# Kernel optimization log

Hardware: AMD Instinct MI355X
Metric: run time of the kernel (lower is better)

## Reference

```python
import jax, jax.numpy as jnp
import numpy as np

B, C, N, F_IN = 8, 5, 512, 768
H, D_HID, D_OUT = 4, 128, 64
NEG_SLOPE = 0.2


def _gat_layer(h, mask, W, a_l, a_r, b, apply_relu):
    # h: [B,N,Fin], mask: [B,N,N] bool (mask[b,i,j]=True means edge i->j)
    Bn, Nn, _ = h.shape
    Hh, Dd = a_l.shape
    feat = (h @ W).reshape(Bn, Nn, Hh, Dd)              # [B,N,H,D]
    el = jnp.einsum('bnhd,hd->bnh', feat, a_l)          # src scores
    er = jnp.einsum('bnhd,hd->bnh', feat, a_r)          # dst scores
    e = jax.nn.leaky_relu(el[:, :, None, :] + er[:, None, :, :], NEG_SLOPE)  # [B,src,dst,H]
    m = mask[..., None]
    e = jnp.where(m, e, jnp.finfo(e.dtype).min)
    emax = jnp.max(e, axis=1, keepdims=True)
    p = jnp.where(m, jnp.exp(e - emax), 0.0)
    s = jnp.sum(p, axis=1, keepdims=True)
    alpha = p / jnp.maximum(s, 1e-9)                    # edge softmax over incoming edges per dst
    out = jnp.einsum('bijh,bihd->bjhd', alpha, feat)    # aggregate src features to dst
    out = out + b.reshape(1, 1, Hh, Dd)
    if apply_relu:
        out = jax.nn.relu(out)
    return out                                           # [B,N,H,D]


def setup_inputs() -> dict:
    key = jax.random.key(0)
    ks = jax.random.split(key, 16)
    x = jax.random.normal(ks[0], (B, C, N, F_IN), dtype=jnp.float32)
    adj = (jax.random.uniform(ks[1], (B, C, N, N)) < 0.1).astype(jnp.float32)
    node_nums = jnp.full((B,), N, dtype=jnp.int32)
    s = 0.02
    W0 = jax.random.normal(ks[2], (C, F_IN, H * D_HID)) * s
    al0 = jax.random.normal(ks[3], (C, H, D_HID)) * s
    ar0 = jax.random.normal(ks[4], (C, H, D_HID)) * s
    b0 = jnp.zeros((C, H * D_HID), jnp.float32)
    W1 = jax.random.normal(ks[5], (C, H * D_HID, H * D_HID)) * s
    al1 = jax.random.normal(ks[6], (C, H, D_HID)) * s
    ar1 = jax.random.normal(ks[7], (C, H, D_HID)) * s
    b1 = jnp.zeros((C, H * D_HID), jnp.float32)
    W2 = jax.random.normal(ks[8], (C, H * D_HID, H * D_OUT)) * s
    al2 = jax.random.normal(ks[9], (C, H, D_OUT)) * s
    ar2 = jax.random.normal(ks[10], (C, H, D_OUT)) * s
    b2 = jnp.zeros((C, H * D_OUT), jnp.float32)
    return dict(x=x, adj=adj, W0=W0, al0=al0, ar0=ar0, b0=b0,
                W1=W1, al1=al1, ar1=ar1, b1=b1,
                W2=W2, al2=al2, ar2=ar2, b2=b2, node_nums=node_nums)


def reference(x, adj, W0, al0, ar0, b0, W1, al1, ar1, b1, W2, al2, ar2, b2, node_nums):
    # Original concatenates per-batch node slices and takes channel 0 features only.
    h0 = x[:, 0]                       # [B,N,F_IN]
    logits_all = []
    for c in range(C):
        mask = adj[:, c] > 0           # [B,N,N]
        h = _gat_layer(h0, mask, W0[c], al0[c], ar0[c], b0[c].reshape(H, D_HID), True).reshape(B, N, H * D_HID)
        h = _gat_layer(h, mask, W1[c], al1[c], ar1[c], b1[c].reshape(H, D_HID), True).reshape(B, N, H * D_HID)
        out = _gat_layer(h, mask, W2[c], al2[c], ar2[c], b2[c].reshape(H, D_OUT), False).mean(axis=2)  # [B,N,D_OUT]
        logits_all.append(out)
    return jnp.concatenate(logits_all, axis=-1)  # [B,N,C*D_OUT]
```

## Files before the change

kernel.cpp:

```cpp
#include <hip/hip_runtime.h>

typedef unsigned int uint;
typedef unsigned short ushort_t;
typedef __attribute__((ext_vector_type(8))) short short8;
typedef __attribute__((ext_vector_type(4))) float f32x4;

#define NB 8
#define NC 5
#define NN 512
#define FIN 768
#define NH 4
#define MT 4096

__device__ __forceinline__ float b2f(ushort_t u){ uint x = ((uint)u)<<16; return __builtin_bit_cast(float, x); }
__device__ __forceinline__ ushort_t f2b(float f){
  uint u = __builtin_bit_cast(uint, f);
  u += 0x7FFFu + ((u>>16)&1u);
  return (ushort_t)(u>>16);
}
__device__ __forceinline__ ushort_t f2b_fast(float f){
  uint u = __builtin_bit_cast(uint, f);
  return (ushort_t)((u + 0x8000u)>>16);
}

#define GLL16(gp, lp) __builtin_amdgcn_global_load_lds( \
    (const __attribute__((address_space(1))) void*)(gp), \
    (__attribute__((address_space(3))) void*)(lp), 16, 0, 0)

__global__ __launch_bounds__(256) void prep(const float* __restrict__ x, ushort_t* __restrict__ h0b,
                                            const float* __restrict__ W0, ushort_t* __restrict__ Wt0,
                                            const float* __restrict__ W1, ushort_t* __restrict__ Wt1,
                                            const float* __restrict__ W2, ushort_t* __restrict__ Wt2,
                                            const float* __restrict__ adj, uint* __restrict__ adjB){
  __shared__ float tile[32][33];
  int bid = blockIdx.x, t = threadIdx.x;
  if (bid < 3072){
    int tid = bid*256 + t;
    int row = tid/192, q = tid%192;
    int b = row >> 9, n = row & 511;
    float4 v = *(const float4*)(x + ((size_t)(b*NC)*NN + n)*FIN + q*4);
    ushort4 o; o.x = f2b(v.x); o.y = f2b(v.y); o.z = f2b(v.z); o.w = f2b(v.w);
    *(ushort4*)(h0b + (size_t)row*FIN + q*4) = o;
  } else if (bid < 6912){
    const float* W; ushort_t* Wt; int K, N, c, x0, y0;
    if (bid < 4992){ int l = bid-3072; K=768; N=512; W=W0; Wt=Wt0; c=l/384; int r=l%384; x0=r%16; y0=r/16; }
    else if (bid < 6272){ int l = bid-4992; K=512; N=512; W=W1; Wt=Wt1; c=l/256; int r=l%256; x0=r%16; y0=r/16; }
    else { int l = bid-6272; K=512; N=256; W=W2; Wt=Wt2; c=l/128; int r=l%128; x0=r%8; y0=r/8; }
    int n0 = x0*32, k0 = y0*32;
    int tx = t & 31, ty = t >> 5;
    const float* Wp = W + (size_t)c*K*N;
    ushort_t* Wtp = Wt + (size_t)c*K*N;
    #pragma unroll
    for (int r=0;r<4;r++) tile[ty+r*8][tx] = Wp[(size_t)(k0+ty+r*8)*N + n0+tx];
    __syncthreads();
    #pragma unroll
    for (int r=0;r<4;r++) Wtp[(size_t)(n0+ty+r*8)*K + k0+tx] = f2b(tile[tx][ty+r*8]);
  } else {
    int l = bid - 6912;
    int iw = l & 15, zz = l >> 4;
    const float* ap = adj + (size_t)zz*NN*NN + (size_t)iw*32*NN;
    uint w0 = 0, w1 = 0;
    #pragma unroll 8
    for (int q=0;q<32;q++){
      if (ap[(size_t)q*NN + t]       > 0.f) w0 |= (1u<<q);
      if (ap[(size_t)q*NN + t + 256] > 0.f) w1 |= (1u<<q);
    }
    adjB[((size_t)zz*16 + iw)*512 + t]       = w0;
    adjB[((size_t)zz*16 + iw)*512 + t + 256] = w1;
  }
}

template<int DH>
__global__ __launch_bounds__(256) void gemm_tn(const ushort_t* __restrict__ A,
                                               const ushort_t* __restrict__ Bt,
                                               ushort_t* __restrict__ Ob,
                                               const float* __restrict__ al, const float* __restrict__ ar,
                                               float* __restrict__ el, float* __restrict__ E1, float* __restrict__ E2,
                                               float* __restrict__ er, float* __restrict__ R1, float* __restrict__ R2,
                                               int K, long a_cs, long b_cs){
  constexpr int DT = NH*DH;
  __shared__ __align__(16) char smem[128*136*2];
  __shared__ float als_s[128], ars_s[128];
  ushort_t* As = (ushort_t*)smem;
  ushort_t* Bs = As + 128*32;
  ushort_t* St = (ushort_t*)smem;
  int c = blockIdx.z;
  const ushort_t* Ap = A + (size_t)c*a_cs;
  const ushort_t* Bp = Bt + (size_t)c*b_cs;
  int m0 = blockIdx.y*128, n0 = blockIdx.x*128;
  int t = threadIdx.x, lane = t & 63, w = t >> 6;
  int l15 = lane & 15, quad = lane >> 4;
  int wm = (w & 1)*64, wn = (w >> 1)*64;
  if (t < 128){
    als_s[t] = al[(size_t)c*NH*DH + n0 + t];
    ars_s[t] = ar[(size_t)c*NH*DH + n0 + t];
  }
  f32x4 acc[4][4] = {};
  for (int k0 = 0; k0 < K; k0 += 32){
    __syncthreads();
    {
      int i = t;
      GLL16(Ap + (size_t)(m0 + (i>>2))*K + k0 + (i&3)*8, As + (size_t)(w*64)*8);
      GLL16(Bp + (size_t)(n0 + (i>>2))*K + k0 + (i&3)*8, Bs + (size_t)(w*64)*8);
      i = t + 256;
      GLL16(Ap + (size_t)(m0 + (i>>2))*K + k0 + (i&3)*8, As + (size_t)(w*64 + 256)*8);
      GLL16(Bp + (size_t)(n0 + (i>>2))*K + k0 + (i&3)*8, Bs + (size_t)(w*64 + 256)*8);
    }
    __syncthreads();
    short8 af[4], bfr[4];
    #pragma unroll
    for (int im=0; im<4; im++) af[im] = *(const short8*)(As + (size_t)(wm + im*16 + l15)*32 + quad*8);
    #pragma unroll
    for (int in=0; in<4; in++) bfr[in] = *(const short8*)(Bs + (size_t)(wn + in*16 + l15)*32 + quad*8);
    #pragma unroll
    for (int im=0; im<4; im++)
      #pragma unroll
      for (int in=0; in<4; in++)
        acc[im][in] = __builtin_amdgcn_mfma_f32_16x16x32_bf16(af[im], bfr[in], acc[im][in], 0, 0, 0);
  }
  __syncthreads();
  #pragma unroll
  for (int im=0; im<4; im++)
    #pragma unroll
    for (int in=0; in<4; in++){
      int n = wn + in*16 + l15;
      #pragma unroll
      for (int r=0; r<4; r++){
        int m = wm + im*16 + quad*4 + r;
        St[(size_t)n*136 + m] = f2b(acc[im][in][r]);
      }
    }
  __syncthreads();
  {
    int n_loc = t >> 1, half = t & 1;
    const ushort_t* srcp = St + (size_t)n_loc*136 + half*64;
    ushort_t* dstc = Ob + (size_t)c*MT*DT;
    #pragma unroll
    for (int q=0;q<8;q++){
      size_t g = (size_t)(m0>>3) + half*8 + q;
      *(short8*)(dstc + (g*DT + n0 + n_loc)*8) = *(const short8*)(srcp + q*8);
    }
  }
  {
    int m = t >> 1, half = t & 1;
    float sl = 0.f, sr = 0.f;
    const ushort_t* stp = St + (size_t)(half*64)*136 + m;
    #pragma unroll 8
    for (int nn=0; nn<64; nn++){
      float f = b2f(stp[(size_t)nn*136]);
      int n = half*64 + nn;
      sl += f*als_s[n]; sr += f*ars_s[n];
    }
    size_t base = (size_t)c*NH*MT;
    if (DH == 128){
      sl += __shfl_xor(sl, 1); sr += __shfl_xor(sr, 1);
      size_t idx = base + (size_t)(n0>>7)*MT + m0 + m;
      if (half == 0){ el[idx]=sl; E1[idx]=__expf(sl); E2[idx]=__expf(0.2f*sl); }
      else          { er[idx]=sr; R1[idx]=__expf(sr); R2[idx]=__expf(0.2f*sr); }
    } else {
      size_t idx = base + (size_t)((n0>>6)+half)*MT + m0 + m;
      el[idx]=sl; E1[idx]=__expf(sl); E2[idx]=__expf(0.2f*sl);
      er[idx]=sr; R1[idx]=__expf(sr); R2[idx]=__expf(0.2f*sr);
    }
  }
}

template<int DH, int RELU>
__global__ __launch_bounds__(256,4) void agg(const ushort_t* __restrict__ featB,
                                             const uint* __restrict__ adjB,
                                             const float* __restrict__ el, const float* __restrict__ E1,
                                             const float* __restrict__ E2,
                                             const float* __restrict__ er, const float* __restrict__ R1,
                                             const float* __restrict__ R2,
                                             const float* __restrict__ bias,
                                             ushort_t* __restrict__ outp){
  constexpr int DT = NH*DH;
  constexpr int BN = DH/16;
  __shared__ __align__(16) ushort_t Fs[2][8*DH*8];
  __shared__ float el_s[512], E1_s[512], E2_s[512];
  int bid = blockIdx.x;
  int g = bid % 160, jt = bid / 160;
  int c = g>>5, b = (g>>2)&7, h = g&3;
  int zz = b*NC + c;
  int j0 = jt*64;
  int t = threadIdx.x, lane = t&63, w = t>>6, l15 = lane&15, quad = lane>>4;
  size_t eb = (size_t)(c*NH + h)*MT + b*NN;
  const ushort_t* fBc = featB + ((size_t)(c*512 + b*64)*DT + h*DH)*8;
  el_s[t] = el[eb + t]; el_s[t+256] = el[eb + t+256];
  E1_s[t] = E1[eb + t]; E1_s[t+256] = E1[eb + t+256];
  E2_s[t] = E2[eb + t]; E2_s[t+256] = E2[eb + t+256];
  int jme = j0 + w*16 + l15;
  float erv = er[eb + jme];
  float R1v = R1[eb + jme];
  float R2v = R2[eb + jme];
  uint mw[16];
  #pragma unroll
  for (int iw=0; iw<16; iw++) mw[iw] = adjB[((size_t)zz*16 + iw)*512 + jme];
  short8 onesv;
  #pragma unroll
  for (int q=0;q<8;q++) onesv[q] = (short)0x3F80;
  f32x4 acc[BN] = {};
  f32x4 accs = {0.f,0.f,0.f,0.f};
  #pragma unroll
  for (int u=0; u<DH/32; u++){
    int gi = w*(DH/32)+u, isub = gi/(DH/64), part = gi%(DH/64);
    GLL16(fBc + (size_t)isub*DT*8 + part*512 + lane*8, &Fs[0][isub*(DH*8) + part*512]);
  }
  __syncthreads();
  for (int ic = 0; ic < 8; ic++){
    int buf = ic & 1;
    if (ic < 7){
      #pragma unroll
      for (int u=0; u<DH/32; u++){
        int gi = w*(DH/32)+u, isub = gi/(DH/64), part = gi%(DH/64);
        GLL16(fBc + (size_t)((ic+1)*8+isub)*DT*8 + part*512 + lane*8, &Fs[buf^1][isub*(DH*8) + part*512]);
      }
    }
    #pragma unroll
    for (int st=0; st<2; st++){
      int i0c = ic*64 + st*32;
      uint mby = (mw[i0c>>5] >> (quad*8)) & 0xFFu;
      float4 ea  = *(const float4*)&el_s[i0c + quad*8];
      float4 eb4 = *(const float4*)&el_s[i0c + quad*8 + 4];
      float4 x1a = *(const float4*)&E1_s[i0c + quad*8];
      float4 x1b = *(const float4*)&E1_s[i0c + quad*8 + 4];
      float4 x2a = *(const float4*)&E2_s[i0c + quad*8];
      float4 x2b = *(const float4*)&E2_s[i0c + quad*8 + 4];
      float ev[8]  = {ea.x,ea.y,ea.z,ea.w,eb4.x,eb4.y,eb4.z,eb4.w};
      float e1v[8] = {x1a.x,x1a.y,x1a.z,x1a.w,x1b.x,x1b.y,x1b.z,x1b.w};
      float e2v[8] = {x2a.x,x2a.y,x2a.z,x2a.w,x2b.x,x2b.y,x2b.z,x2b.w};
      short8 af;
      #pragma unroll
      for (int q=0;q<8;q++){
        float s = ev[q] + erv;
        float p = (s > 0.f) ? (e1v[q]*R1v) : (e2v[q]*R2v);
        p = ((mby>>q)&1u) ? p : 0.f;
        af[q] = (short)f2b_fast(p);
      }
      accs = __builtin_amdgcn_mfma_f32_16x16x32_bf16(af, onesv, accs, 0, 0, 0);
      #pragma unroll
      for (int in=0; in<BN; in++){
        short8 bfr = *(const short8*)&Fs[buf][(st*4+quad)*(DH*8) + (in*16+l15)*8];
        acc[in] = __builtin_amdgcn_mfma_f32_16x16x32_bf16(af, bfr, acc[in], 0, 0, 0);
      }
    }
    __syncthreads();
  }
  ushort_t* op = outp + ((size_t)c*MT + b*NN + j0 + w*16)*DT + h*DH;
  float bv[BN];
  #pragma unroll
  for (int in=0; in<BN; in++) bv[in] = bias[(size_t)c*DT + h*DH + in*16 + l15];
  #pragma unroll
  for (int r=0; r<4; r++){
    int jr = quad*4 + r;
    float sinv = 1.f / fmaxf(accs[r], 1e-9f);
    #pragma unroll
    for (int in=0; in<BN; in++){
      float o = acc[in][r]*sinv + bv[in];
      if (RELU) o = fmaxf(o, 0.f);
      op[(size_t)jr*DT + in*16 + l15] = f2b_fast(o);
    }
  }
}

__global__ __launch_bounds__(256) void meank(const ushort_t* __restrict__ h2, float* __restrict__ outp){
  int tid = blockIdx.x*256 + threadIdx.x;
  if (tid >= MT*NC*64) return;
  int d = tid & 63; int r = tid >> 6; int c = r % NC; int m = r / NC;
  const ushort_t* p = h2 + ((size_t)c*MT + m)*256 + d;
  float s = 0.25f*(b2f(p[0]) + b2f(p[64]) + b2f(p[128]) + b2f(p[192]));
  outp[(size_t)m*(NC*64) + c*64 + d] = s;
}

extern "C" void kernel_launch(void* const* d_in, const int* in_sizes, int n_in,
                              void* d_out, int out_size, void* d_ws, size_t ws_size,
                              hipStream_t stream){
  const float* x   = (const float*)d_in[0];
  const float* adj = (const float*)d_in[1];
  const float* W0  = (const float*)d_in[2];
  const float* al0 = (const float*)d_in[3];
  const float* ar0 = (const float*)d_in[4];
  const float* b0  = (const float*)d_in[5];
  const float* W1  = (const float*)d_in[6];
  const float* al1 = (const float*)d_in[7];
  const float* ar1 = (const float*)d_in[8];
  const float* b1  = (const float*)d_in[9];
  const float* W2  = (const float*)d_in[10];
  const float* al2 = (const float*)d_in[11];
  const float* ar2 = (const float*)d_in[12];
  const float* b2  = (const float*)d_in[13];

  ushort_t* h0b  = (ushort_t*)d_ws;
  ushort_t* Wt0  = h0b  + (size_t)MT*FIN;
  ushort_t* Wt1  = Wt0  + (size_t)5*512*768;
  ushort_t* Wt2  = Wt1  + (size_t)5*512*512;
  ushort_t* featB= Wt2  + (size_t)5*256*512;
  ushort_t* hnat = featB+ (size_t)5*(size_t)MT*512;
  uint*     adjB = (uint*)(hnat + (size_t)5*(size_t)MT*512);
  float*    elp  = (float*)(adjB + (size_t)40*16*512);
  float*    E1p  = elp + (size_t)NC*NH*MT;
  float*    E2p  = E1p + (size_t)NC*NH*MT;
  float*    erp  = E2p + (size_t)NC*NH*MT;
  float*    R1p  = erp + (size_t)NC*NH*MT;
  float*    R2p  = R1p + (size_t)NC*NH*MT;

  prep<<<7552, 256, 0, stream>>>(x, h0b, W0, Wt0, W1, Wt1, W2, Wt2, adj, adjB);

  gemm_tn<128><<<dim3(4,32,5), 256, 0, stream>>>(h0b, Wt0, featB, al0, ar0,
                                                 elp, E1p, E2p, erp, R1p, R2p,
                                                 768, 0L, (long)512*768);
  agg<128,1><<<1280, 256, 0, stream>>>(featB, adjB, elp, E1p, E2p, erp, R1p, R2p, b0, hnat);
  gemm_tn<128><<<dim3(4,32,5), 256, 0, stream>>>(hnat, Wt1, featB, al1, ar1,
                                                 elp, E1p, E2p, erp, R1p, R2p,
                                                 512, (long)MT*512, (long)512*512);
  agg<128,1><<<1280, 256, 0, stream>>>(featB, adjB, elp, E1p, E2p, erp, R1p, R2p, b1, hnat);
  gemm_tn<64><<<dim3(2,32,5), 256, 0, stream>>>(hnat, Wt2, featB, al2, ar2,
                                                elp, E1p, E2p, erp, R1p, R2p,
                                                512, (long)MT*512, (long)256*512);
  agg<64,0><<<1280, 256, 0, stream>>>(featB, adjB, elp, E1p, E2p, erp, R1p, R2p, b2, hnat);

  meank<<<5120, 256, 0, stream>>>(hnat, (float*)d_out);
}
```

Measured before the change: 303.7 us.

## Double destination rows per agg block to reuse feature tiles, stage mask in LDS

Each aggregation block now covers 128 destination nodes instead of 64, with each wave computing two 16-row MFMA tiles. This reuses each loaded source-feature tile twice, halving global feature traffic and the grid size. The adjacency mask words are staged in shared memory instead of registers, and bf16 packing uses a hardware pack-convert builtin when available. In exchange, per-thread accumulator registers double and the launch-bounds occupancy hint is dropped, which may lower occupancy. The grid also shrinks to 640 blocks.

```diff
diff --git a/kernel.cpp b/kernel.cpp
--- a/kernel.cpp
+++ b/kernel.cpp
@@ -22,6 +22,17 @@
   uint u = __builtin_bit_cast(uint, f);
   return (ushort_t)((u + 0x8000u)>>16);
 }
+
+#if __has_builtin(__builtin_amdgcn_cvt_pk_bf16_f32)
+typedef __bf16 bf16x2 __attribute__((ext_vector_type(2)));
+__device__ __forceinline__ uint pk2(float a, float b){
+  return __builtin_bit_cast(uint, __builtin_amdgcn_cvt_pk_bf16_f32(a, b));
+}
+#else
+__device__ __forceinline__ uint pk2(float a, float b){
+  return (uint)f2b_fast(a) | ((uint)f2b_fast(b) << 16);
+}
+#endif
 
 #define GLL16(gp, lp) __builtin_amdgcn_global_load_lds( \
     (const __attribute__((address_space(1))) void*)(gp), \
@@ -166,41 +177,46 @@
 }
 
 template<int DH, int RELU>
-__global__ __launch_bounds__(256,4) void agg(const ushort_t* __restrict__ featB,
-                                             const uint* __restrict__ adjB,
-                                             const float* __restrict__ el, const float* __restrict__ E1,
-                                             const float* __restrict__ E2,
-                                             const float* __restrict__ er, const float* __restrict__ R1,
-                                             const float* __restrict__ R2,
-                                             const float* __restrict__ bias,
-                                             ushort_t* __restrict__ outp){
+__global__ __launch_bounds__(256) void agg(const ushort_t* __restrict__ featB,
+                                           const uint* __restrict__ adjB,
+                                           const float* __restrict__ el, const float* __restrict__ E1,
+                                           const float* __restrict__ E2,
+                                           const float* __restrict__ er, const float* __restrict__ R1,
+                                           const float* __restrict__ R2,
+                                           const float* __restrict__ bias,
+                                           ushort_t* __restrict__ outp){
   constexpr int DT = NH*DH;
   constexpr int BN = DH/16;
   __shared__ __align__(16) ushort_t Fs[2][8*DH*8];
   __shared__ float el_s[512], E1_s[512], E2_s[512];
+  __shared__ uint Ms[16*128];
   int bid = blockIdx.x;
   int g = bid % 160, jt = bid / 160;
   int c = g>>5, b = (g>>2)&7, h = g&3;
   int zz = b*NC + c;
-  int j0 = jt*64;
+  int j0 = jt*128;
   int t = threadIdx.x, lane = t&63, w = t>>6, l15 = lane&15, quad = lane>>4;
   size_t eb = (size_t)(c*NH + h)*MT + b*NN;
   const ushort_t* fBc = featB + ((size_t)(c*512 + b*64)*DT + h*DH)*8;
   el_s[t] = el[eb + t]; el_s[t+256] = el[eb + t+256];
   E1_s[t] = E1[eb + t]; E1_s[t+256] = E1[eb + t+256];
   E2_s[t] = E2[eb + t]; E2_s[t+256] = E2[eb + t+256];
-  int jme = j0 + w*16 + l15;
-  float erv = er[eb + jme];
-  float R1v = R1[eb + jme];
-  float R2v = R2[eb + jme];
-  uint mw[16];
-  #pragma unroll
-  for (int iw=0; iw<16; iw++) mw[iw] = adjB[((size_t)zz*16 + iw)*512 + jme];
+  #pragma unroll
+  for (int k=0;k<8;k++){
+    int idx = k*256 + t;
+    Ms[idx] = adjB[((size_t)zz*16 + (idx>>7))*512 + j0 + (idx&127)];
+  }
+  float erv[2], R1v[2], R2v[2];
+  #pragma unroll
+  for (int im=0; im<2; im++){
+    int jme = j0 + w*32 + im*16 + l15;
+    erv[im] = er[eb + jme]; R1v[im] = R1[eb + jme]; R2v[im] = R2[eb + jme];
+  }
   short8 onesv;
   #pragma unroll
   for (int q=0;q<8;q++) onesv[q] = (short)0x3F80;
-  f32x4 acc[BN] = {};
-  f32x4 accs = {0.f,0.f,0.f,0.f};
+  f32x4 acc[2][BN] = {};
+  f32x4 accs[2] = {};
   #pragma unroll
   for (int u=0; u<DH/32; u++){
     int gi = w*(DH/32)+u, isub = gi/(DH/64), part = gi%(DH/64);
@@ -219,7 +235,7 @@
     #pragma unroll
     for (int st=0; st<2; st++){
       int i0c = ic*64 + st*32;
-      uint mby = (mw[i0c>>5] >> (quad*8)) & 0xFFu;
+      int iw = i0c >> 5;
       float4 ea  = *(const float4*)&el_s[i0c + quad*8];
       float4 eb4 = *(const float4*)&el_s[i0c + quad*8 + 4];
       float4 x1a = *(const float4*)&E1_s[i0c + quad*8];
@@ -229,36 +245,50 @@
       float ev[8]  = {ea.x,ea.y,ea.z,ea.w,eb4.x,eb4.y,eb4.z,eb4.w};
       float e1v[8] = {x1a.x,x1a.y,x1a.z,x1a.w,x1b.x,x1b.y,x1b.z,x1b.w};
       float e2v[8] = {x2a.x,x2a.y,x2a.z,x2a.w,x2b.x,x2b.y,x2b.z,x2b.w};
-      short8 af;
-      #pragma unroll
-      for (int q=0;q<8;q++){
-        float s = ev[q] + erv;
-        float p = (s > 0.f) ? (e1v[q]*R1v) : (e2v[q]*R2v);
-        p = ((mby>>q)&1u) ? p : 0.f;
-        af[q] = (short)f2b_fast(p);
+      short8 bfr[BN];
+      #pragma unroll
+      for (int in=0; in<BN; in++)
+        bfr[in] = *(const short8*)&Fs[buf][(st*4+quad)*(DH*8) + (in*16+l15)*8];
+      #pragma unroll
+      for (int im=0; im<2; im++){
+        uint mby = (Ms[iw*128 + w*32 + im*16 + l15] >> (quad*8)) & 0xFFu;
+        float pv[8];
+        #pragma unroll
+        for (int q=0;q<8;q++){
+          float s  = ev[q] + erv[im];
+          float Ei = (s > 0.f) ? e1v[q] : e2v[q];
+          float Rv = (s > 0.f) ? R1v[im] : R2v[im];
+          float p  = Ei*Rv;
+          pv[q] = ((mby>>q)&1u) ? p : 0.f;
+        }
+        uint4 pw;
+        pw.x = pk2(pv[0], pv[1]); pw.y = pk2(pv[2], pv[3]);
+        pw.z = pk2(pv[4], pv[5]); pw.w = pk2(pv[6], pv[7]);
+        short8 af = __builtin_bit_cast(short8, pw);
+        accs[im] = __builtin_amdgcn_mfma_f32_16x16x32_bf16(af, onesv, accs[im], 0, 0, 0);
+        #pragma unroll
+        for (int in=0; in<BN; in++)
+          acc[im][in] = __builtin_amdgcn_mfma_f32_16x16x32_bf16(af, bfr[in], acc[im][in], 0, 0, 0);
       }
-      accs = __builtin_amdgcn_mfma_f32_16x16x32_bf16(af, onesv, accs, 0, 0, 0);
+    }
+    __syncthreads();
+  }
+  ushort_t* op = outp + ((size_t)c*MT + b*NN + j0 + w*32)*DT + h*DH;
+  float bv[BN];
+  #pragma unroll
+  for (int in=0; in<BN; in++) bv[in] = bias[(size_t)c*DT + h*DH + in*16 + l15];
+  #pragma unroll
+  for (int im=0; im<2; im++){
+    #pragma unroll
+    for (int r=0; r<4; r++){
+      int jr = im*16 + quad*4 + r;
+      float sinv = 1.f / fmaxf(accs[im][r], 1e-9f);
       #pragma unroll
       for (int in=0; in<BN; in++){
-        short8 bfr = *(const short8*)&Fs[buf][(st*4+quad)*(DH*8) + (in*16+l15)*8];
-        acc[in] = __builtin_amdgcn_mfma_f32_16x16x32_bf16(af, bfr, acc[in], 0, 0, 0);
+        float o = acc[im][in][r]*sinv + bv[in];
+        if (RELU) o = fmaxf(o, 0.f);
+        op[(size_t)jr*DT + in*16 + l15] = f2b_fast(o);
       }
-    }
-    __syncthreads();
-  }
-  ushort_t* op = outp + ((size_t)c*MT + b*NN + j0 + w*16)*DT + h*DH;
-  float bv[BN];
-  #pragma unroll
-  for (int in=0; in<BN; in++) bv[in] = bias[(size_t)c*DT + h*DH + in*16 + l15];
-  #pragma unroll
-  for (int r=0; r<4; r++){
-    int jr = quad*4 + r;
-    float sinv = 1.f / fmaxf(accs[r], 1e-9f);
-    #pragma unroll
-    for (int in=0; in<BN; in++){
-      float o = acc[in][r]*sinv + bv[in];
-      if (RELU) o = fmaxf(o, 0.f);
-      op[(size_t)jr*DT + in*16 + l15] = f2b_fast(o);
     }
   }
 }
@@ -309,15 +339,15 @@
   gemm_tn<128><<<dim3(4,32,5), 256, 0, stream>>>(h0b, Wt0, featB, al0, ar0,
                                                  elp, E1p, E2p, erp, R1p, R2p,
                                                  768, 0L, (long)512*768);
-  agg<128,1><<<1280, 256, 0, stream>>>(featB, adjB, elp, E1p, E2p, erp, R1p, R2p, b0, hnat);
+  agg<128,1><<<640, 256, 0, stream>>>(featB, adjB, elp, E1p, E2p, erp, R1p, R2p, b0, hnat);
   gemm_tn<128><<<dim3(4,32,5), 256, 0, stream>>>(hnat, Wt1, featB, al1, ar1,
                                                  elp, E1p, E2p, erp, R1p, R2p,
                                                  512, (long)MT*512, (long)512*512);
-  agg<128,1><<<1280, 256, 0, stream>>>(featB, adjB, elp, E1p, E2p, erp, R1p, R2p, b1, hnat);
+  agg<128,1><<<640, 256, 0, stream>>>(featB, adjB, elp, E1p, E2p, erp, R1p, R2p, b1, hnat);
   gemm_tn<64><<<dim3(2,32,5), 256, 0, stream>>>(hnat, Wt2, featB, al2, ar2,
                                                 elp, E1p, E2p, erp, R1p, R2p,
                                                 512, (long)MT*512, (long)256*512);
-  agg<64,0><<<1280, 256, 0, stream>>>(featB, adjB, elp, E1p, E2p, erp, R1p, R2p, b2, hnat);
+  agg<64,0><<<640, 256, 0, stream>>>(featB, adjB, elp, E1p, E2p, erp, R1p, R2p, b2, hnat);
 
   meank<<<5120, 256, 0, stream>>>(hnat, (float*)d_out);
 }
```

After: 330.0 us. 1.09x slower.

## Halve agg LDS stage size, stage adjacency mask in LDS, raise occupancy

Applied to the files above, without the earlier changes.

The agg kernel now double-buffers 32 source rows per stage instead of 64, running 16 iterations instead of 8. This halves the feature LDS footprint. The 16 per-thread adjacency mask words move from registers into a shared-memory array, and launch bounds rise from 4 to 5 blocks per CU. The aim is lower register and LDS pressure so more waves are resident. It also adds a packed bf16 conversion builtin and batches B-fragment loads ahead of the MFMAs. The cost is twice as many barriers and an extra LDS read per iteration.

```diff
diff --git a/kernel.cpp b/kernel.cpp
--- a/kernel.cpp
+++ b/kernel.cpp
@@ -22,6 +22,17 @@
   uint u = __builtin_bit_cast(uint, f);
   return (ushort_t)((u + 0x8000u)>>16);
 }
+
+#if __has_builtin(__builtin_amdgcn_cvt_pk_bf16_f32)
+typedef __bf16 bf16x2 __attribute__((ext_vector_type(2)));
+__device__ __forceinline__ uint pk2(float a, float b){
+  return __builtin_bit_cast(uint, __builtin_amdgcn_cvt_pk_bf16_f32(a, b));
+}
+#else
+__device__ __forceinline__ uint pk2(float a, float b){
+  return (uint)f2b_fast(a) | ((uint)f2b_fast(b) << 16);
+}
+#endif
 
 #define GLL16(gp, lp) __builtin_amdgcn_global_load_lds( \
     (const __attribute__((address_space(1))) void*)(gp), \
@@ -166,7 +177,7 @@
 }
 
 template<int DH, int RELU>
-__global__ __launch_bounds__(256,4) void agg(const ushort_t* __restrict__ featB,
+__global__ __launch_bounds__(256,5) void agg(const ushort_t* __restrict__ featB,
                                              const uint* __restrict__ adjB,
                                              const float* __restrict__ el, const float* __restrict__ E1,
                                              const float* __restrict__ E2,
@@ -176,8 +187,9 @@
                                              ushort_t* __restrict__ outp){
   constexpr int DT = NH*DH;
   constexpr int BN = DH/16;
-  __shared__ __align__(16) ushort_t Fs[2][8*DH*8];
+  __shared__ __align__(16) ushort_t Fs[2][4*DH*8];
   __shared__ float el_s[512], E1_s[512], E2_s[512];
+  __shared__ uint Ms[16*64];
   int bid = blockIdx.x;
   int g = bid % 160, jt = bid / 160;
   int c = g>>5, b = (g>>2)&7, h = g&3;
@@ -189,60 +201,65 @@
   el_s[t] = el[eb + t]; el_s[t+256] = el[eb + t+256];
   E1_s[t] = E1[eb + t]; E1_s[t+256] = E1[eb + t+256];
   E2_s[t] = E2[eb + t]; E2_s[t+256] = E2[eb + t+256];
+  #pragma unroll
+  for (int k=0;k<4;k++){
+    int idx = k*256 + t;
+    Ms[idx] = adjB[((size_t)zz*16 + (idx>>6))*512 + j0 + (idx&63)];
+  }
   int jme = j0 + w*16 + l15;
   float erv = er[eb + jme];
   float R1v = R1[eb + jme];
   float R2v = R2[eb + jme];
-  uint mw[16];
-  #pragma unroll
-  for (int iw=0; iw<16; iw++) mw[iw] = adjB[((size_t)zz*16 + iw)*512 + jme];
   short8 onesv;
   #pragma unroll
   for (int q=0;q<8;q++) onesv[q] = (short)0x3F80;
   f32x4 acc[BN] = {};
   f32x4 accs = {0.f,0.f,0.f,0.f};
   #pragma unroll
-  for (int u=0; u<DH/32; u++){
-    int gi = w*(DH/32)+u, isub = gi/(DH/64), part = gi%(DH/64);
-    GLL16(fBc + (size_t)isub*DT*8 + part*512 + lane*8, &Fs[0][isub*(DH*8) + part*512]);
-  }
+  for (int part=0; part<DH/64; part++)
+    GLL16(fBc + (size_t)w*DT*8 + part*512 + lane*8, &Fs[0][w*(DH*8) + part*512]);
   __syncthreads();
-  for (int ic = 0; ic < 8; ic++){
+  for (int ic = 0; ic < 16; ic++){
     int buf = ic & 1;
-    if (ic < 7){
-      #pragma unroll
-      for (int u=0; u<DH/32; u++){
-        int gi = w*(DH/32)+u, isub = gi/(DH/64), part = gi%(DH/64);
-        GLL16(fBc + (size_t)((ic+1)*8+isub)*DT*8 + part*512 + lane*8, &Fs[buf^1][isub*(DH*8) + part*512]);
-      }
-    }
-    #pragma unroll
-    for (int st=0; st<2; st++){
-      int i0c = ic*64 + st*32;
-      uint mby = (mw[i0c>>5] >> (quad*8)) & 0xFFu;
-      float4 ea  = *(const float4*)&el_s[i0c + quad*8];
-      float4 eb4 = *(const float4*)&el_s[i0c + quad*8 + 4];
-      float4 x1a = *(const float4*)&E1_s[i0c + quad*8];
-      float4 x1b = *(const float4*)&E1_s[i0c + quad*8 + 4];
-      float4 x2a = *(const float4*)&E2_s[i0c + quad*8];
-      float4 x2b = *(const float4*)&E2_s[i0c + quad*8 + 4];
-      float ev[8]  = {ea.x,ea.y,ea.z,ea.w,eb4.x,eb4.y,eb4.z,eb4.w};
-      float e1v[8] = {x1a.x,x1a.y,x1a.z,x1a.w,x1b.x,x1b.y,x1b.z,x1b.w};
-      float e2v[8] = {x2a.x,x2a.y,x2a.z,x2a.w,x2b.x,x2b.y,x2b.z,x2b.w};
-      short8 af;
-      #pragma unroll
-      for (int q=0;q<8;q++){
-        float s = ev[q] + erv;
-        float p = (s > 0.f) ? (e1v[q]*R1v) : (e2v[q]*R2v);
-        p = ((mby>>q)&1u) ? p : 0.f;
-        af[q] = (short)f2b_fast(p);
-      }
-      accs = __builtin_amdgcn_mfma_f32_16x16x32_bf16(af, onesv, accs, 0, 0, 0);
-      #pragma unroll
-      for (int in=0; in<BN; in++){
-        short8 bfr = *(const short8*)&Fs[buf][(st*4+quad)*(DH*8) + (in*16+l15)*8];
-        acc[in] = __builtin_amdgcn_mfma_f32_16x16x32_bf16(af, bfr, acc[in], 0, 0, 0);
-      }
+    if (ic < 15){
+      #pragma unroll
+      for (int part=0; part<DH/64; part++)
+        GLL16(fBc + (size_t)((ic+1)*4+w)*DT*8 + part*512 + lane*8, &Fs[buf^1][w*(DH*8) + part*512]);
+    }
+    int i0c = ic*32;
+    uint mby = (Ms[ic*64 + w*16 + l15] >> (quad*8)) & 0xFFu;
+    float4 ea  = *(const float4*)&el_s[i0c + quad*8];
+    float4 eb4 = *(const float4*)&el_s[i0c + quad*8 + 4];
+    float4 x1a = *(const float4*)&E1_s[i0c + quad*8];
+    float4 x1b = *(const float4*)&E1_s[i0c + quad*8 + 4];
+    float4 x2a = *(const float4*)&E2_s[i0c + quad*8];
+    float4 x2b = *(const float4*)&E2_s[i0c + quad*8 + 4];
+    float ev[8]  = {ea.x,ea.y,ea.z,ea.w,eb4.x,eb4.y,eb4.z,eb4.w};
+    float e1v[8] = {x1a.x,x1a.y,x1a.z,x1a.w,x1b.x,x1b.y,x1b.z,x1b.w};
+    float e2v[8] = {x2a.x,x2a.y,x2a.z,x2a.w,x2b.x,x2b.y,x2b.z,x2b.w};
+    float pv[8];
+    #pragma unroll
+    for (int q=0;q<8;q++){
+      float s  = ev[q] + erv;
+      float Ei = (s > 0.f) ? e1v[q] : e2v[q];
+      float Rv = (s > 0.f) ? R1v : R2v;
+      float p  = Ei*Rv;
+      pv[q] = ((mby>>q)&1u) ? p : 0.f;
+    }
+    uint4 pw;
+    pw.x = pk2(pv[0], pv[1]); pw.y = pk2(pv[2], pv[3]);
+    pw.z = pk2(pv[4], pv[5]); pw.w = pk2(pv[6], pv[7]);
+    short8 af = __builtin_bit_cast(short8, pw);
+    accs = __builtin_amdgcn_mfma_f32_16x16x32_bf16(af, onesv, accs, 0, 0, 0);
+    #pragma unroll
+    for (int half=0; half<2; half++){
+      short8 bfr[BN/2];
+      #pragma unroll
+      for (int in=0; in<BN/2; in++)
+        bfr[in] = *(const short8*)&Fs[buf][quad*(DH*8) + ((half*(BN/2)+in)*16 + l15)*8];
+      #pragma unroll
+      for (int in=0; in<BN/2; in++)
+        acc[half*(BN/2)+in] = __builtin_amdgcn_mfma_f32_16x16x32_bf16(af, bfr[in], acc[half*(BN/2)+in], 0, 0, 0);
     }
     __syncthreads();
   }
```

Result: no change. 300.3 us (-1.1%).
